# Kernel tuning notes

Measured on AMD Instinct MI355X. Metric: run time of the kernel, lower is better.

## Reference

```python
import jax, jax.numpy as jnp
import numpy as np

RADIUS = 0.1      # ball-query radius; also max_dist in collision_error
THRESH = 0.001    # collision threshold
NSAMPLE = 4       # neighbors per query point
EPS = 1e-7
LOSS_WEIGHT = 1.0


def _face_normals(verts, faces):
    # verts: (b, n_v, 3), faces: (b, n_f, 3) int -> unit face normals (b, n_f, 3)
    tri = jax.vmap(lambda V, F: V[F])(verts, faces)  # (b, n_f, 3verts, 3xyz)
    e1 = tri[:, :, 1] - tri[:, :, 0]
    e2 = tri[:, :, 2] - tri[:, :, 0]
    fn = jnp.cross(e1, e2)
    return fn / (jnp.linalg.norm(fn, axis=-1, keepdims=True) + EPS)


def _vertex_normals(faces, fn, n_v):
    # sparse v2f bmm equivalent: average incident face normals per vertex
    def scatter(F, N):
        idx = F.reshape(-1)                    # (3*n_f,) face->vertex ids
        vals = jnp.repeat(N, 3, axis=0)        # each face normal to its 3 verts
        s = jnp.zeros((n_v, 3), N.dtype).at[idx].add(vals)
        c = jnp.zeros((n_v, 1), N.dtype).at[idx].add(jnp.float32(1.0))
        return s / (c + EPS)
    return jax.vmap(scatter)(faces, fn)        # (b, n_v, 3)


def _ball_query(new_xyz, xyz, radius, nsample):
    # PointNet++ ball query: first `nsample` points of xyz within radius of each
    # new_xyz point; unfilled slots repeat the first hit (0 if no hits).
    d2 = jnp.sum((new_xyz[:, :, None, :] - xyz[:, None, :, :]) ** 2, axis=-1)  # (b, nq, nv)
    within = d2 < radius * radius
    c = jnp.cumsum(within.astype(jnp.int32), axis=-1)
    n_within = c[..., -1]
    first_idx = jnp.argmax(within, axis=-1)    # 0 when no hits (matches CUDA kernel)
    slots = []
    for j in range(nsample):
        idx_j = jnp.argmax(within & (c == j + 1), axis=-1)
        slots.append(jnp.where(n_within > j, idx_j, first_idx))
    return jnp.stack(slots, axis=-1)           # (b, nq, nsample)


def _collision_loss(pred, h_state, h_faces):
    faces = jnp.swapaxes(h_faces, 1, 2)                 # (b, n_f, 3)
    human_verts = jnp.swapaxes(h_state, 1, 2)[..., :3]  # (b, n_v, 3)
    n_v = human_verts.shape[1]

    fn = _face_normals(human_verts, faces)
    vn = _vertex_normals(faces, fn, n_v)                # (b, n_v, 3)

    idx = _ball_query(pred, human_verts, RADIUS, NSAMPLE)      # (b, nq, K)
    gxyz = jax.vmap(lambda V, I: V[I])(human_verts, idx)       # (b, nq, K, 3)
    gn = jax.vmap(lambda V, I: V[I])(vn, idx)                  # (b, nq, K, 3)

    diff = pred[:, :, None, :] - gxyz
    gn = gn / (jnp.linalg.norm(gn, axis=-1, keepdims=True) + EPS)
    dot = jnp.sum(diff * gn, axis=-1)                   # (b, nq, K)
    valid_dot = (dot - THRESH) * (dot >= -RADIUS)       # max_dist = radius
    mask = valid_dot < 0
    per_pt = jnp.sum(valid_dot * mask / (jnp.sum(mask, axis=-1, keepdims=True) + EPS), axis=-1) ** 2
    avg_mask = per_pt > 0
    loss = jnp.sum(per_pt)                              # reduction='sum', weight=None
    loss = loss / (jnp.sum(avg_mask) + EPS)
    return LOSS_WEIGHT * loss


def setup_inputs() -> dict:
    key = jax.random.key(0)
    k1, k2, k3, k4 = jax.random.split(key, 4)
    bs, n_pred, n_v, n_f, C = 2, 8192, 6890, 13776, 6
    pred = jax.random.uniform(k1, (bs, n_pred, 3), dtype=jnp.float32)
    label = jax.random.uniform(k2, (bs, n_pred, 3), dtype=jnp.float32)
    h_state = jax.random.uniform(k3, (bs, C, n_v), dtype=jnp.float32)
    h_faces = jax.random.randint(k4, (bs, 3, n_f), 0, n_v, dtype=jnp.int32)
    return {"pred": pred, "label": label, "h_state": h_state, "h_faces": h_faces}


def reference(pred, label, h_state, h_faces):
    # label is unused by collision_error (kept for signature fidelity)
    return _collision_loss(pred, h_state, h_faces)
```

## Files before the change

### kernel.cpp

```cpp
#include <hip/hip_runtime.h>
#include <cstdint>

#define EPSF 1e-7f

__global__ void face_scatter_kernel(const float* __restrict__ hs,
                                    const int* __restrict__ hf,
                                    float* __restrict__ svec,
                                    float* __restrict__ scnt,
                                    int n_v, int n_f, int bs) {
    int t = blockIdx.x * blockDim.x + threadIdx.x;
    if (t >= bs * n_f) return;
    int b = t / n_f;
    int f = t - b * n_f;
    const int* fb = hf + (size_t)b * 3 * n_f;
    int i0 = fb[f];
    int i1 = fb[n_f + f];
    int i2 = fb[2 * n_f + f];
    const float* xs = hs + (size_t)b * 6 * n_v;
    const float* ys = xs + n_v;
    const float* zs = xs + 2 * n_v;
    float ax = xs[i0], ay = ys[i0], az = zs[i0];
    float bx = xs[i1], by = ys[i1], bz = zs[i1];
    float cx = xs[i2], cy = ys[i2], cz = zs[i2];
    float e1x = bx - ax, e1y = by - ay, e1z = bz - az;
    float e2x = cx - ax, e2y = cy - ay, e2z = cz - az;
    float fx = e1y * e2z - e1z * e2y;
    float fy = e1z * e2x - e1x * e2z;
    float fz = e1x * e2y - e1y * e2x;
    float nrm = sqrtf(fx * fx + fy * fy + fz * fz) + EPSF;
    fx /= nrm; fy /= nrm; fz /= nrm;
    float* sb = svec + (size_t)b * n_v * 3;
    float* cb = scnt + (size_t)b * n_v;
    int idx3[3] = {i0, i1, i2};
    #pragma unroll
    for (int k = 0; k < 3; ++k) {
        int i = idx3[k];
        atomicAdd(&sb[i * 3 + 0], fx);
        atomicAdd(&sb[i * 3 + 1], fy);
        atomicAdd(&sb[i * 3 + 2], fz);
        atomicAdd(&cb[i], 1.0f);
    }
}

__global__ void vertex_normal_kernel(float* __restrict__ svec,
                                     const float* __restrict__ scnt,
                                     int total) {
    int t = blockIdx.x * blockDim.x + threadIdx.x;
    if (t >= total) return;
    float cc = scnt[t] + EPSF;
    float vx = svec[t * 3 + 0] / cc;
    float vy = svec[t * 3 + 1] / cc;
    float vz = svec[t * 3 + 2] / cc;
    float nrm = sqrtf(vx * vx + vy * vy + vz * vz) + EPSF;
    svec[t * 3 + 0] = vx / nrm;
    svec[t * 3 + 1] = vy / nrm;
    svec[t * 3 + 2] = vz / nrm;
}

__global__ void query_loss_kernel(const float* __restrict__ pred,
                                  const float* __restrict__ hs,
                                  const float* __restrict__ un,
                                  double* __restrict__ partial,
                                  float* __restrict__ pcnt,
                                  int n_v, int n_pred, int bs) {
    const int lane = threadIdx.x & 63;
    const int wave = threadIdx.x >> 6;
    const int wid = blockIdx.x * 4 + wave;
    const int nq = bs * n_pred;

    float per_pt = 0.0f;
    float is_pos = 0.0f;

    if (wid < nq) {
        const int b = wid / n_pred;
        const int q = wid - b * n_pred;
        const float* xs = hs + (size_t)b * 6 * n_v;
        const float* ys = xs + n_v;
        const float* zs = xs + 2 * n_v;
        const float* unb = un + (size_t)b * n_v * 3;
        const float px = pred[((size_t)b * n_pred + q) * 3 + 0];
        const float py = pred[((size_t)b * n_pred + q) * 3 + 1];
        const float pz = pred[((size_t)b * n_pred + q) * 3 + 2];

        int found = 0;
        int h0 = 0, h1 = 0, h2 = 0, h3 = 0;
        const int nchunks = (n_v + 63) >> 6;
        for (int c = 0; c < nchunks; ++c) {
            int v = (c << 6) + lane;
            int vc = v < n_v ? v : (n_v - 1);
            float dx = px - xs[vc];
            float dy = py - ys[vc];
            float dz = pz - zs[vc];
            float d2 = dx * dx + dy * dy + dz * dz;
            bool within = (v < n_v) && (d2 < 0.01f);
            unsigned long long m = __ballot(within);
            while (m != 0ull && found < 4) {
                int bit = __builtin_ctzll(m);
                int vid = (c << 6) + bit;
                if (found == 0)      h0 = vid;
                else if (found == 1) h1 = vid;
                else if (found == 2) h2 = vid;
                else                 h3 = vid;
                ++found;
                m &= m - 1;
            }
            if (found >= 4) break;
        }

        int id0 = h0;
        int id1 = (found > 1) ? h1 : h0;
        int id2 = (found > 2) ? h2 : h0;
        int id3 = (found > 3) ? h3 : h0;
        int ids[4] = {id0, id1, id2, id3};

        float vd[4];
        float cm = 0.0f;
        #pragma unroll
        for (int j = 0; j < 4; ++j) {
            int id = ids[j];
            float dx = px - xs[id];
            float dy = py - ys[id];
            float dz = pz - zs[id];
            float nx = unb[id * 3 + 0];
            float ny = unb[id * 3 + 1];
            float nz = unb[id * 3 + 2];
            float dot = dx * nx + dy * ny + dz * nz;
            float w = (dot >= -0.1f) ? 1.0f : 0.0f;
            float v = (dot - 0.001f) * w;
            bool msk = v < 0.0f;
            vd[j] = msk ? v : 0.0f;
            cm += msk ? 1.0f : 0.0f;
        }
        float s = ((vd[0] + vd[1]) + vd[2]) + vd[3];
        float a = s / (cm + EPSF);
        per_pt = a * a;
        is_pos = (per_pt > 0.0f) ? 1.0f : 0.0f;
    }

    __shared__ float ls[4];
    __shared__ float lc[4];
    if (lane == 0) { ls[wave] = per_pt; lc[wave] = is_pos; }
    __syncthreads();
    if (threadIdx.x == 0) {
        double ssum = (double)ls[0] + (double)ls[1] + (double)ls[2] + (double)ls[3];
        float csum = ((lc[0] + lc[1]) + lc[2]) + lc[3];
        partial[blockIdx.x] = ssum;
        pcnt[blockIdx.x] = csum;
    }
}

__global__ void finalize_kernel(const double* __restrict__ partial,
                                const float* __restrict__ pcnt,
                                int n, float* __restrict__ out) {
    double s = 0.0, c = 0.0;
    for (int i = threadIdx.x; i < n; i += blockDim.x) {
        s += partial[i];
        c += (double)pcnt[i];
    }
    #pragma unroll
    for (int off = 32; off > 0; off >>= 1) {
        s += __shfl_down(s, off);
        c += __shfl_down(c, off);
    }
    __shared__ double ws_s[4];
    __shared__ double ws_c[4];
    int wave = threadIdx.x >> 6;
    int lane = threadIdx.x & 63;
    if (lane == 0) { ws_s[wave] = s; ws_c[wave] = c; }
    __syncthreads();
    if (threadIdx.x == 0) {
        double S = ws_s[0] + ws_s[1] + ws_s[2] + ws_s[3];
        double C = ws_c[0] + ws_c[1] + ws_c[2] + ws_c[3];
        out[0] = (float)(S / (C + 1e-7));
    }
}

extern "C" void kernel_launch(void* const* d_in, const int* in_sizes, int n_in,
                              void* d_out, int out_size, void* d_ws, size_t ws_size,
                              hipStream_t stream) {
    const float* pred    = (const float*)d_in[0];
    const float* h_state = (const float*)d_in[2];
    const int*   h_faces = (const int*)d_in[3];
    float* out = (float*)d_out;

    const int bs = 2;
    const int n_pred = in_sizes[0] / (bs * 3);
    const int n_v    = in_sizes[2] / (bs * 6);
    const int n_f    = in_sizes[3] / (bs * 3);

    float* svec = (float*)d_ws;
    float* scnt = svec + (size_t)bs * n_v * 3;
    size_t off_f = (size_t)bs * n_v * 4;
    off_f = (off_f + 1) & ~(size_t)1;
    const int nq = bs * n_pred;
    const int nblk = (nq + 3) / 4;
    double* partial = (double*)(svec + off_f);
    float*  pcnt    = (float*)(partial + nblk);

    hipMemsetAsync(d_ws, 0, (size_t)bs * n_v * 4 * sizeof(float), stream);

    int t1 = bs * n_f;
    face_scatter_kernel<<<(t1 + 255) / 256, 256, 0, stream>>>(
        h_state, h_faces, svec, scnt, n_v, n_f, bs);

    int t2 = bs * n_v;
    vertex_normal_kernel<<<(t2 + 255) / 256, 256, 0, stream>>>(svec, scnt, t2);

    query_loss_kernel<<<nblk, 256, 0, stream>>>(
        pred, h_state, svec, partial, pcnt, n_v, n_pred, bs);

    finalize_kernel<<<1, 256, 0, stream>>>(partial, pcnt, nblk, out);
}
```

Baseline: 119.7 us.

## Replace brute-force ball query with uniform grid spatial binning

Bins the mesh vertices into a fixed 10x10x10 grid over the unit cube with one cell per radius, using a count, a scan and a scatter into packed float4 records. Each query wave then scans only the neighbouring cell rows instead of streaming all vertices. Lane-local sorted top-4 lists plus wave min-reductions keep the first-by-index semantics of the ball query. The separate finalize kernel becomes a last-block reduction inside the query kernel. In exchange it adds extra kernels and atomics for building the grid, and the fixed grid only prunes well when the coordinates lie roughly in [0,1].

```diff
diff --git a/kernel.cpp b/kernel.cpp
--- a/kernel.cpp
+++ b/kernel.cpp
@@ -1,68 +1,141 @@
 #include <hip/hip_runtime.h>
 #include <cstdint>
+#include <climits>
 
 #define EPSF 1e-7f
-
-__global__ void face_scatter_kernel(const float* __restrict__ hs,
-                                    const int* __restrict__ hf,
-                                    float* __restrict__ svec,
-                                    float* __restrict__ scnt,
-                                    int n_v, int n_f, int bs) {
+#define NCELL 1000
+#define RPAD 0.10002f
+
+__device__ __forceinline__ int cell_of(float x, float y, float z) {
+    int cx = min(max((int)(x * 10.0f), 0), 9);
+    int cy = min(max((int)(y * 10.0f), 0), 9);
+    int cz = min(max((int)(z * 10.0f), 0), 9);
+    return (cx * 10 + cy) * 10 + cz;
+}
+
+__global__ void k1_face_count(const float* __restrict__ hs,
+                              const int* __restrict__ hf,
+                              float* __restrict__ svec,
+                              float* __restrict__ scnt,
+                              int* __restrict__ counts,
+                              int n_v, int n_f, int bs) {
     int t = blockIdx.x * blockDim.x + threadIdx.x;
-    if (t >= bs * n_f) return;
-    int b = t / n_f;
-    int f = t - b * n_f;
-    const int* fb = hf + (size_t)b * 3 * n_f;
-    int i0 = fb[f];
-    int i1 = fb[n_f + f];
-    int i2 = fb[2 * n_f + f];
+    if (t < bs * n_f) {
+        int b = t / n_f;
+        int f = t - b * n_f;
+        const int* fb = hf + (size_t)b * 3 * n_f;
+        int i0 = fb[f];
+        int i1 = fb[n_f + f];
+        int i2 = fb[2 * n_f + f];
+        const float* xs = hs + (size_t)b * 6 * n_v;
+        const float* ys = xs + n_v;
+        const float* zs = xs + 2 * n_v;
+        float ax = xs[i0], ay = ys[i0], az = zs[i0];
+        float bx = xs[i1], by = ys[i1], bz = zs[i1];
+        float cx = xs[i2], cy = ys[i2], cz = zs[i2];
+        float e1x = bx - ax, e1y = by - ay, e1z = bz - az;
+        float e2x = cx - ax, e2y = cy - ay, e2z = cz - az;
+        float fx = e1y * e2z - e1z * e2y;
+        float fy = e1z * e2x - e1x * e2z;
+        float fz = e1x * e2y - e1y * e2x;
+        float nrm = sqrtf(fx * fx + fy * fy + fz * fz) + EPSF;
+        fx /= nrm; fy /= nrm; fz /= nrm;
+        float* sb = svec + (size_t)b * n_v * 3;
+        float* cb = scnt + (size_t)b * n_v;
+        int idx3[3] = {i0, i1, i2};
+        #pragma unroll
+        for (int k = 0; k < 3; ++k) {
+            int i = idx3[k];
+            atomicAdd(&sb[i * 3 + 0], fx);
+            atomicAdd(&sb[i * 3 + 1], fy);
+            atomicAdd(&sb[i * 3 + 2], fz);
+            atomicAdd(&cb[i], 1.0f);
+        }
+    }
+    if (t < bs * n_v) {
+        int b = t / n_v;
+        int v = t - b * n_v;
+        const float* xs = hs + (size_t)b * 6 * n_v;
+        float x = xs[v], y = xs[n_v + v], z = xs[2 * n_v + v];
+        atomicAdd(&counts[b * NCELL + cell_of(x, y, z)], 1);
+    }
+}
+
+__global__ void k2_vn_scan(float* __restrict__ svec,
+                           const float* __restrict__ scnt,
+                           const int* __restrict__ counts,
+                           int* __restrict__ cellstart,
+                           int* __restrict__ cursor,
+                           int total_v, int nvb) {
+    if (blockIdx.x < (unsigned)nvb) {
+        int t = blockIdx.x * blockDim.x + threadIdx.x;
+        if (t >= total_v) return;
+        float cc = scnt[t] + EPSF;
+        float vx = svec[t * 3 + 0] / cc;
+        float vy = svec[t * 3 + 1] / cc;
+        float vz = svec[t * 3 + 2] / cc;
+        float nrm = sqrtf(vx * vx + vy * vy + vz * vz) + EPSF;
+        svec[t * 3 + 0] = vx / nrm;
+        svec[t * 3 + 1] = vy / nrm;
+        svec[t * 3 + 2] = vz / nrm;
+        return;
+    }
+    if (threadIdx.x >= 128) return;
+    int batch = threadIdx.x >> 6;
+    int lane = threadIdx.x & 63;
+    int local[16];
+    int mysum = 0;
+    #pragma unroll
+    for (int k = 0; k < 16; ++k) {
+        int c = lane * 16 + k;
+        int v = (c < NCELL) ? counts[batch * NCELL + c] : 0;
+        local[k] = v;
+        mysum += v;
+    }
+    int s = mysum;
+    #pragma unroll
+    for (int off = 1; off < 64; off <<= 1) {
+        int n = __shfl_up(s, off);
+        if (lane >= off) s += n;
+    }
+    int excl = s - mysum;
+    #pragma unroll
+    for (int k = 0; k < 16; ++k) {
+        int c = lane * 16 + k;
+        if (c < NCELL) {
+            cellstart[batch * (NCELL + 1) + c] = excl;
+            cursor[batch * NCELL + c] = excl;
+            excl += local[k];
+        }
+    }
+    if (lane == 63) cellstart[batch * (NCELL + 1) + NCELL] = s;
+}
+
+__global__ void k3_scatter(const float* __restrict__ hs,
+                           int* __restrict__ cursor,
+                           float4* __restrict__ spk,
+                           int n_v, int bs) {
+    int t = blockIdx.x * blockDim.x + threadIdx.x;
+    if (t >= bs * n_v) return;
+    int b = t / n_v;
+    int v = t - b * n_v;
     const float* xs = hs + (size_t)b * 6 * n_v;
-    const float* ys = xs + n_v;
-    const float* zs = xs + 2 * n_v;
-    float ax = xs[i0], ay = ys[i0], az = zs[i0];
-    float bx = xs[i1], by = ys[i1], bz = zs[i1];
-    float cx = xs[i2], cy = ys[i2], cz = zs[i2];
-    float e1x = bx - ax, e1y = by - ay, e1z = bz - az;
-    float e2x = cx - ax, e2y = cy - ay, e2z = cz - az;
-    float fx = e1y * e2z - e1z * e2y;
-    float fy = e1z * e2x - e1x * e2z;
-    float fz = e1x * e2y - e1y * e2x;
-    float nrm = sqrtf(fx * fx + fy * fy + fz * fz) + EPSF;
-    fx /= nrm; fy /= nrm; fz /= nrm;
-    float* sb = svec + (size_t)b * n_v * 3;
-    float* cb = scnt + (size_t)b * n_v;
-    int idx3[3] = {i0, i1, i2};
-    #pragma unroll
-    for (int k = 0; k < 3; ++k) {
-        int i = idx3[k];
-        atomicAdd(&sb[i * 3 + 0], fx);
-        atomicAdd(&sb[i * 3 + 1], fy);
-        atomicAdd(&sb[i * 3 + 2], fz);
-        atomicAdd(&cb[i], 1.0f);
-    }
-}
-
-__global__ void vertex_normal_kernel(float* __restrict__ svec,
-                                     const float* __restrict__ scnt,
-                                     int total) {
-    int t = blockIdx.x * blockDim.x + threadIdx.x;
-    if (t >= total) return;
-    float cc = scnt[t] + EPSF;
-    float vx = svec[t * 3 + 0] / cc;
-    float vy = svec[t * 3 + 1] / cc;
-    float vz = svec[t * 3 + 2] / cc;
-    float nrm = sqrtf(vx * vx + vy * vy + vz * vz) + EPSF;
-    svec[t * 3 + 0] = vx / nrm;
-    svec[t * 3 + 1] = vy / nrm;
-    svec[t * 3 + 2] = vz / nrm;
-}
-
-__global__ void query_loss_kernel(const float* __restrict__ pred,
-                                  const float* __restrict__ hs,
-                                  const float* __restrict__ un,
-                                  double* __restrict__ partial,
-                                  float* __restrict__ pcnt,
-                                  int n_v, int n_pred, int bs) {
+    float x = xs[v], y = xs[n_v + v], z = xs[2 * n_v + v];
+    int cell = cell_of(x, y, z);
+    int pos = atomicAdd(&cursor[b * NCELL + cell], 1);
+    spk[(size_t)b * n_v + pos] = make_float4(x, y, z, __int_as_float(v));
+}
+
+__global__ void k4_query(const float* __restrict__ pred,
+                         const float* __restrict__ hs,
+                         const float* __restrict__ un,
+                         const float4* __restrict__ spk,
+                         const int* __restrict__ cellstart,
+                         double* __restrict__ partial,
+                         float* __restrict__ pcnt,
+                         int* __restrict__ done,
+                         float* __restrict__ out,
+                         int n_v, int n_pred, int bs) {
     const int lane = threadIdx.x & 63;
     const int wave = threadIdx.x >> 6;
     const int wid = blockIdx.x * 4 + wave;
@@ -73,44 +146,65 @@
 
     if (wid < nq) {
         const int b = wid / n_pred;
-        const int q = wid - b * n_pred;
         const float* xs = hs + (size_t)b * 6 * n_v;
         const float* ys = xs + n_v;
         const float* zs = xs + 2 * n_v;
         const float* unb = un + (size_t)b * n_v * 3;
-        const float px = pred[((size_t)b * n_pred + q) * 3 + 0];
-        const float py = pred[((size_t)b * n_pred + q) * 3 + 1];
-        const float pz = pred[((size_t)b * n_pred + q) * 3 + 2];
-
-        int found = 0;
-        int h0 = 0, h1 = 0, h2 = 0, h3 = 0;
-        const int nchunks = (n_v + 63) >> 6;
-        for (int c = 0; c < nchunks; ++c) {
-            int v = (c << 6) + lane;
-            int vc = v < n_v ? v : (n_v - 1);
-            float dx = px - xs[vc];
-            float dy = py - ys[vc];
-            float dz = pz - zs[vc];
-            float d2 = dx * dx + dy * dy + dz * dz;
-            bool within = (v < n_v) && (d2 < 0.01f);
-            unsigned long long m = __ballot(within);
-            while (m != 0ull && found < 4) {
-                int bit = __builtin_ctzll(m);
-                int vid = (c << 6) + bit;
-                if (found == 0)      h0 = vid;
-                else if (found == 1) h1 = vid;
-                else if (found == 2) h2 = vid;
-                else                 h3 = vid;
-                ++found;
-                m &= m - 1;
+        const float4* sp = spk + (size_t)b * n_v;
+        const int* csb = cellstart + b * (NCELL + 1);
+        const float px = pred[(size_t)wid * 3 + 0];
+        const float py = pred[(size_t)wid * 3 + 1];
+        const float pz = pred[(size_t)wid * 3 + 2];
+
+        int xlo = max(0, (int)floorf((px - RPAD) * 10.0f));
+        int xhi = min(9, (int)floorf((px + RPAD) * 10.0f));
+        int ylo = max(0, (int)floorf((py - RPAD) * 10.0f));
+        int yhi = min(9, (int)floorf((py + RPAD) * 10.0f));
+        int zlo = max(0, (int)floorf((pz - RPAD) * 10.0f));
+        int zhi = min(9, (int)floorf((pz + RPAD) * 10.0f));
+
+        int l0 = INT_MAX, l1 = INT_MAX, l2 = INT_MAX, l3 = INT_MAX;
+        for (int cx = xlo; cx <= xhi; ++cx) {
+            for (int cy = ylo; cy <= yhi; ++cy) {
+                int rowbase = (cx * 10 + cy) * 10;
+                int rs = csb[rowbase + zlo];
+                int re = csb[rowbase + zhi + 1];
+                for (int p = rs + lane; p < re; p += 64) {
+                    float4 c4 = sp[p];
+                    float dx = px - c4.x;
+                    float dy = py - c4.y;
+                    float dz = pz - c4.z;
+                    float d2 = dx * dx + dy * dy + dz * dz;
+                    if (d2 < 0.01f) {
+                        int vid = __float_as_int(c4.w);
+                        if (vid < l3) {
+                            if (vid < l1) {
+                                if (vid < l0) { l3 = l2; l2 = l1; l1 = l0; l0 = vid; }
+                                else          { l3 = l2; l2 = l1; l1 = vid; }
+                            } else {
+                                if (vid < l2) { l3 = l2; l2 = vid; }
+                                else          { l3 = vid; }
+                            }
+                        }
+                    }
+                }
             }
-            if (found >= 4) break;
-        }
-
-        int id0 = h0;
-        int id1 = (found > 1) ? h1 : h0;
-        int id2 = (found > 2) ? h2 : h0;
-        int id3 = (found > 3) ? h3 : h0;
+        }
+
+        int a0 = l0, a1 = l1, a2 = l2, a3 = l3;
+        int s0, s1, s2, s3;
+        #pragma unroll
+        for (int j = 0; j < 4; ++j) {
+            int m = a0;
+            #pragma unroll
+            for (int off = 1; off < 64; off <<= 1) m = min(m, __shfl_xor(m, off));
+            if (j == 0) s0 = m; else if (j == 1) s1 = m; else if (j == 2) s2 = m; else s3 = m;
+            if (a0 == m && m != INT_MAX) { a0 = a1; a1 = a2; a2 = a3; a3 = INT_MAX; }
+        }
+        int id0 = (s0 == INT_MAX) ? 0 : s0;
+        int id1 = (s1 == INT_MAX) ? id0 : s1;
+        int id2 = (s2 == INT_MAX) ? id0 : s2;
+        int id3 = (s3 == INT_MAX) ? id0 : s3;
         int ids[4] = {id0, id1, id2, id3};
 
         float vd[4];
@@ -142,36 +236,34 @@
     if (lane == 0) { ls[wave] = per_pt; lc[wave] = is_pos; }
     __syncthreads();
     if (threadIdx.x == 0) {
-        double ssum = (double)ls[0] + (double)ls[1] + (double)ls[2] + (double)ls[3];
-        float csum = ((lc[0] + lc[1]) + lc[2]) + lc[3];
-        partial[blockIdx.x] = ssum;
-        pcnt[blockIdx.x] = csum;
-    }
-}
-
-__global__ void finalize_kernel(const double* __restrict__ partial,
-                                const float* __restrict__ pcnt,
-                                int n, float* __restrict__ out) {
-    double s = 0.0, c = 0.0;
-    for (int i = threadIdx.x; i < n; i += blockDim.x) {
-        s += partial[i];
-        c += (double)pcnt[i];
-    }
-    #pragma unroll
-    for (int off = 32; off > 0; off >>= 1) {
-        s += __shfl_down(s, off);
-        c += __shfl_down(c, off);
-    }
-    __shared__ double ws_s[4];
-    __shared__ double ws_c[4];
-    int wave = threadIdx.x >> 6;
-    int lane = threadIdx.x & 63;
-    if (lane == 0) { ws_s[wave] = s; ws_c[wave] = c; }
+        partial[blockIdx.x] = (double)ls[0] + (double)ls[1] + (double)ls[2] + (double)ls[3];
+        pcnt[blockIdx.x] = ((lc[0] + lc[1]) + lc[2]) + lc[3];
+    }
+    __threadfence();
+    __shared__ int lastflag;
+    if (threadIdx.x == 0) lastflag = (atomicAdd(done, 1) == (int)gridDim.x - 1) ? 1 : 0;
     __syncthreads();
-    if (threadIdx.x == 0) {
-        double S = ws_s[0] + ws_s[1] + ws_s[2] + ws_s[3];
-        double C = ws_c[0] + ws_c[1] + ws_c[2] + ws_c[3];
-        out[0] = (float)(S / (C + 1e-7));
+    if (lastflag) {
+        __threadfence();
+        double s = 0.0, c = 0.0;
+        for (int i = threadIdx.x; i < (int)gridDim.x; i += blockDim.x) {
+            s += partial[i];
+            c += (double)pcnt[i];
+        }
+        #pragma unroll
+        for (int off = 32; off > 0; off >>= 1) {
+            s += __shfl_down(s, off);
+            c += __shfl_down(c, off);
+        }
+        __shared__ double ds[4];
+        __shared__ double dc[4];
+        if (lane == 0) { ds[wave] = s; dc[wave] = c; }
+        __syncthreads();
+        if (threadIdx.x == 0) {
+            double S = ds[0] + ds[1] + ds[2] + ds[3];
+            double C = dc[0] + dc[1] + dc[2] + dc[3];
+            out[0] = (float)(S / (C + 1e-7));
+        }
     }
 }
 
@@ -187,27 +279,45 @@
     const int n_pred = in_sizes[0] / (bs * 3);
     const int n_v    = in_sizes[2] / (bs * 6);
     const int n_f    = in_sizes[3] / (bs * 3);
-
-    float* svec = (float*)d_ws;
-    float* scnt = svec + (size_t)bs * n_v * 3;
-    size_t off_f = (size_t)bs * n_v * 4;
-    off_f = (off_f + 1) & ~(size_t)1;
     const int nq = bs * n_pred;
     const int nblk = (nq + 3) / 4;
-    double* partial = (double*)(svec + off_f);
-    float*  pcnt    = (float*)(partial + nblk);
-
-    hipMemsetAsync(d_ws, 0, (size_t)bs * n_v * 4 * sizeof(float), stream);
+
+    size_t o_svec    = 0;
+    size_t o_scnt    = o_svec + (size_t)bs * n_v * 3;
+    size_t o_counts  = o_scnt + (size_t)bs * n_v;
+    size_t o_done    = o_counts + (size_t)bs * NCELL;
+    size_t o_zeroend = (o_done + 1 + 3) & ~(size_t)3;
+    size_t o_cursor  = o_zeroend;
+    size_t o_cs      = o_cursor + (size_t)bs * NCELL;
+    size_t o_partial = (o_cs + (size_t)bs * (NCELL + 1) + 1) & ~(size_t)1;
+    size_t o_pcnt    = o_partial + 2 * (size_t)nblk;
+    size_t o_spk     = (o_pcnt + (size_t)nblk + 3) & ~(size_t)3;
+
+    float* base = (float*)d_ws;
+    float*  svec      = base + o_svec;
+    float*  scnt      = base + o_scnt;
+    int*    counts    = (int*)(base + o_counts);
+    int*    done      = (int*)(base + o_done);
+    int*    cursor    = (int*)(base + o_cursor);
+    int*    cellstart = (int*)(base + o_cs);
+    double* partial   = (double*)(base + o_partial);
+    float*  pcnt      = base + o_pcnt;
+    float4* spk       = (float4*)(base + o_spk);
+
+    hipMemsetAsync(d_ws, 0, o_zeroend * sizeof(float), stream);
 
     int t1 = bs * n_f;
-    face_scatter_kernel<<<(t1 + 255) / 256, 256, 0, stream>>>(
-        h_state, h_faces, svec, scnt, n_v, n_f, bs);
-
-    int t2 = bs * n_v;
-    vertex_normal_kernel<<<(t2 + 255) / 256, 256, 0, stream>>>(svec, scnt, t2);
-
-    query_loss_kernel<<<nblk, 256, 0, stream>>>(
-        pred, h_state, svec, partial, pcnt, n_v, n_pred, bs);
-
-    finalize_kernel<<<1, 256, 0, stream>>>(partial, pcnt, nblk, out);
-}
+    k1_face_count<<<(t1 + 255) / 256, 256, 0, stream>>>(
+        h_state, h_faces, svec, scnt, counts, n_v, n_f, bs);
+
+    int nvb = (bs * n_v + 255) / 256;
+    k2_vn_scan<<<nvb + 1, 256, 0, stream>>>(
+        svec, scnt, counts, cellstart, cursor, bs * n_v, nvb);
+
+    k3_scatter<<<(bs * n_v + 255) / 256, 256, 0, stream>>>(
+        h_state, cursor, spk, n_v, bs);
+
+    k4_query<<<nblk, 256, 0, stream>>>(
+        pred, h_state, svec, spk, cellstart, partial, pcnt, done, out,
+        n_v, n_pred, bs);
+}
```

After: 427.4 us. 3.57x slower.
